# Optimization experiments

Hardware: AMD Instinct MI355X
Metric: run time of the kernel (lower is better)

The kernel has to match this reference:

```python
import jax, jax.numpy as jnp
import numpy as np

EPS = 1e-6

def _quant_per_token(x):
    # dynamic per-token symmetric int8 quantization (simulated in float)
    s = jnp.max(jnp.abs(x), axis=-1, keepdims=True) / 127.0  # [T,1]
    q = jnp.clip(jnp.round(x / s), -127.0, 127.0)
    return q, s

def _quant_weight(W):
    # per-output-channel symmetric int8 weight quantization (W: [out,in])
    s = jnp.max(jnp.abs(W), axis=1, keepdims=True) / 127.0  # [out,1]
    q = jnp.round(W / s)
    return q, s

def _w8a8(qx, sx, W, b):
    # int8xint8 GEMM with per-token act scale and per-channel weight scale, fp out
    qw, sw = _quant_weight(W)
    return (qx @ qw.T) * (sx * sw.T) + b

def _rmsnorm_bias(x, w, b, eps=EPS):
    # RMSNormGeneral: x * rsqrt(mean(x^2)+eps) * w + b (no mean subtraction)
    var = jnp.mean(x * x, axis=-1, keepdims=True)
    return x * jax.lax.rsqrt(var + eps) * w + b

def setup_inputs() -> dict:
    key = jax.random.key(0)
    ks = jax.random.split(key, 16)
    E, H, F = 1280, 20, 5120
    B, S = 16, 1024
    T = B * S
    d = {
        'hidden': jax.random.normal(ks[0], (T, E), jnp.float32),
        'ln1_w': jax.random.uniform(ks[1], (E,), jnp.float32, 0.5, 1.5),
        'ln1_b': jax.random.normal(ks[2], (E,), jnp.float32) * 0.02,
        'ln2_w': jax.random.uniform(ks[3], (E,), jnp.float32, 0.5, 1.5),
        'ln2_b': jax.random.normal(ks[4], (E,), jnp.float32) * 0.02,
        'W_qkv': jax.random.normal(ks[5], (3 * E, E), jnp.float32) * 0.02,
        'b_qkv': jax.random.normal(ks[6], (3 * E,), jnp.float32) * 0.02,
        'W_out': jax.random.normal(ks[7], (E, E), jnp.float32) * 0.02,
        'b_out': jax.random.normal(ks[8], (E,), jnp.float32) * 0.02,
        'W_fc1': jax.random.normal(ks[9], (F, E), jnp.float32) * 0.02,
        'b_fc1': jax.random.normal(ks[10], (F,), jnp.float32) * 0.02,
        'W_fc2': jax.random.normal(ks[11], (E, F), jnp.float32) * 0.02,
        'b_fc2': jax.random.normal(ks[12], (E,), jnp.float32) * 0.02,
        'bsz': B,
        'seqlen': S,
    }
    return d

def reference(hidden, ln1_w, ln1_b, ln2_w, ln2_b, W_qkv, b_qkv, W_out, b_out,
              W_fc1, b_fc1, W_fc2, b_fc2, bsz, seqlen):
    E = hidden.shape[-1]
    H = 20
    hd = E // H

    # --- self-attention block ---
    residual = hidden
    y = _rmsnorm_bias(hidden, ln1_w, ln1_b)
    qx, sx = _quant_per_token(y)
    qkv = _w8a8(qx, sx, W_qkv, b_qkv)                      # [T, 3E]
    q, k, v = jnp.split(qkv, 3, axis=-1)
    q = q.reshape(bsz, seqlen, H, hd)
    k = k.reshape(bsz, seqlen, H, hd)
    v = v.reshape(bsz, seqlen, H, hd)
    scale = 1.0 / np.sqrt(hd)
    scores = jnp.einsum('bqhd,bkhd->bhqk', q, k) * scale   # non-causal
    probs = jax.nn.softmax(scores, axis=-1)
    attn = jnp.einsum('bhqk,bkhd->bqhd', probs, v).reshape(bsz * seqlen, E)
    qa, sa = _quant_per_token(attn)
    o = _w8a8(qa, sa, W_out, b_out)
    hidden = residual + o

    # --- MLP block ---
    residual = hidden
    y = _rmsnorm_bias(hidden, ln2_w, ln2_b)
    qx, sx = _quant_per_token(y)
    f1 = _w8a8(qx, sx, W_fc1, b_fc1)                       # [T, F]
    g = jax.nn.gelu(f1, approximate=False)                 # fused gelu_and_quant
    qg, sg = _quant_per_token(g)
    f2 = _w8a8(qg, sg, W_fc2, b_fc2)
    return residual + f2
```

## Files before the change

kernel.cpp:

```cpp
#include <hip/hip_runtime.h>
#include <hip/hip_bf16.h>
#include <stdint.h>

#define E_DIM 1280
#define F_DIM 5120
#define T_DIM 16384
#define B_SZ  16
#define S_LEN 1024
#define NH    20

typedef int v4i __attribute__((ext_vector_type(4)));
typedef __attribute__((ext_vector_type(8))) short v8s;
typedef __attribute__((ext_vector_type(4))) float v4f;

__device__ __forceinline__ float wred_sum(float v) {
#pragma unroll
  for (int m = 32; m > 0; m >>= 1) v += __shfl_xor(v, m, 64);
  return v;
}
__device__ __forceinline__ float wred_max(float v) {
#pragma unroll
  for (int m = 32; m > 0; m >>= 1) v = fmaxf(v, __shfl_xor(v, m, 64));
  return v;
}
__device__ __forceinline__ void gload_lds16(const void* g, void* l) {
  __builtin_amdgcn_global_load_lds((const __attribute__((address_space(1))) void*)g,
                                   (__attribute__((address_space(3))) void*)l, 16, 0, 0);
}

__global__ __launch_bounds__(256) void wquant_kernel(
    const float* __restrict__ W, int8_t* __restrict__ qw, float* __restrict__ sw, int K) {
  __shared__ float red[4];
  const int row = blockIdx.x;
  const int tid = threadIdx.x;
  const float* wr = W + (size_t)row * K;
  float amax = 0.f;
  for (int c = tid; c < K; c += 256) amax = fmaxf(amax, fabsf(wr[c]));
  amax = wred_max(amax);
  if ((tid & 63) == 0) red[tid >> 6] = amax;
  __syncthreads();
  amax = fmaxf(fmaxf(red[0], red[1]), fmaxf(red[2], red[3]));
  float sc = amax * (1.0f / 127.0f);
  if (tid == 0) sw[row] = sc;
  for (int c = tid; c < K; c += 256) {
    float qv = rintf(wr[c] / sc);
    qw[(size_t)row * K + c] = (int8_t)qv;
  }
}

__global__ __launch_bounds__(256) void rms_quant_kernel(
    const float* __restrict__ x, const float* __restrict__ w, const float* __restrict__ b,
    int8_t* __restrict__ q, float* __restrict__ s) {
  __shared__ float red[4];
  const int row = blockIdx.x;
  const int tid = threadIdx.x;
  const float* xr = x + (size_t)row * E_DIM;
  float vals[5];
  float ss = 0.f;
#pragma unroll
  for (int i = 0; i < 5; ++i) {
    float v = xr[tid + i * 256];
    vals[i] = v; ss += v * v;
  }
  ss = wred_sum(ss);
  if ((tid & 63) == 0) red[tid >> 6] = ss;
  __syncthreads();
  ss = red[0] + red[1] + red[2] + red[3];
  float rstd = rsqrtf(ss * (1.0f / E_DIM) + 1e-6f);
  float y[5]; float amax = 0.f;
#pragma unroll
  for (int i = 0; i < 5; ++i) {
    int c = tid + i * 256;
    float v = vals[i] * rstd * w[c] + b[c];
    y[i] = v;
    amax = fmaxf(amax, fabsf(v));
  }
  amax = wred_max(amax);
  __syncthreads();
  if ((tid & 63) == 0) red[tid >> 6] = amax;
  __syncthreads();
  amax = fmaxf(fmaxf(red[0], red[1]), fmaxf(red[2], red[3]));
  float sc = amax * (1.0f / 127.0f);
  if (tid == 0) s[row] = sc;
#pragma unroll
  for (int i = 0; i < 5; ++i) {
    int c = tid + i * 256;
    float qv = rintf(y[i] / sc);
    qv = fminf(fmaxf(qv, -127.f), 127.f);
    q[(size_t)row * E_DIM + c] = (int8_t)qv;
  }
}

__global__ __launch_bounds__(256) void row_quant_bf_kernel(
    const __hip_bfloat16* __restrict__ x, int8_t* __restrict__ q, float* __restrict__ s) {
  __shared__ float red[4];
  const int row = blockIdx.x;
  const int tid = threadIdx.x;
  const __hip_bfloat16* xr = x + (size_t)row * E_DIM;
  float vals[5]; float amax = 0.f;
#pragma unroll
  for (int i = 0; i < 5; ++i) {
    float v = __bfloat162float(xr[tid + i * 256]);
    vals[i] = v;
    amax = fmaxf(amax, fabsf(v));
  }
  amax = wred_max(amax);
  if ((tid & 63) == 0) red[tid >> 6] = amax;
  __syncthreads();
  amax = fmaxf(fmaxf(red[0], red[1]), fmaxf(red[2], red[3]));
  float sc = amax * (1.0f / 127.0f);
  if (tid == 0) s[row] = sc;
#pragma unroll
  for (int i = 0; i < 5; ++i) {
    int c = tid + i * 256;
    float qv = rintf(vals[i] / sc);
    qv = fminf(fmaxf(qv, -127.f), 127.f);
    q[(size_t)row * E_DIM + c] = (int8_t)qv;
  }
}

__global__ __launch_bounds__(256) void gelu_quant_kernel(
    const __hip_bfloat16* __restrict__ f1, int8_t* __restrict__ q, float* __restrict__ s) {
  __shared__ float red[4];
  const int row = blockIdx.x;
  const int tid = threadIdx.x;
  const __hip_bfloat16* xr = f1 + (size_t)row * F_DIM;
  float g[20]; float amax = 0.f;
#pragma unroll
  for (int i = 0; i < 20; ++i) {
    float v = __bfloat162float(xr[tid + i * 256]);
    float gv = 0.5f * v * (1.0f + erff(v * 0.70710678118654752440f));
    g[i] = gv;
    amax = fmaxf(amax, fabsf(gv));
  }
  amax = wred_max(amax);
  if ((tid & 63) == 0) red[tid >> 6] = amax;
  __syncthreads();
  amax = fmaxf(fmaxf(red[0], red[1]), fmaxf(red[2], red[3]));
  float sc = amax * (1.0f / 127.0f);
  if (tid == 0) s[row] = sc;
  int8_t* qr = q + (size_t)row * (2 * F_DIM);
#pragma unroll
  for (int i = 0; i < 20; ++i) {
    int c = tid + i * 256;
    float qv = rintf(g[i] / sc);
    qv = fminf(fmaxf(qv, -127.f), 127.f);
    qr[c] = (int8_t)qv;
  }
}

template <int MODE>
__global__ __launch_bounds__(512, 2) void gemm256_i8(
    const int8_t* __restrict__ A, const int8_t* __restrict__ B,
    const float* __restrict__ sx, const float* __restrict__ sw,
    const float* __restrict__ bias, const float* __restrict__ resid,
    void* __restrict__ outp, int M, int N, int K, int lda) {
  __shared__ __align__(16) int8_t As[2][2][256 * 64];
  __shared__ __align__(16) int8_t Bs[2][2][256 * 64];

  const int tid = threadIdx.x;
  const int lane = tid & 63;
  const int wave = tid >> 6;
  const int wm = wave >> 2;
  const int wn = wave & 3;
  const int l16 = lane & 15;
  const int quad = lane >> 4;
  const int choff = (quad ^ ((l16 >> 1) & 3)) << 4;

  const int nwg = gridDim.x;
  const int ntn = N >> 8;
  const int u = (blockIdx.x & 7) * (nwg >> 3) + (blockIdx.x >> 3);
  const int tm = u / ntn, tn = u % ntn;
  const int m0 = tm << 8, n0 = tn << 8;

  const int8_t* A_blk = A + (size_t)m0 * lda;
  const int8_t* B_blk = B + (size_t)n0 * K;

  const int r0 = tid >> 2;
  const int sch = ((tid & 3) ^ ((tid >> 3) & 3)) << 4;

#define STAGE_A(KT, DST)                                                         \
  {                                                                              \
    gload_lds16(A_blk + (size_t)r0 * lda + (size_t)(KT)*64 + sch,                \
                (DST) + tid * 16);                                               \
    gload_lds16(A_blk + (size_t)(r0 + 128) * lda + (size_t)(KT)*64 + sch,        \
                (DST) + 8192 + tid * 16);                                        \
  }
#define STAGE_B(KT, DST)                                                         \
  {                                                                              \
    gload_lds16(B_blk + (size_t)r0 * K + (size_t)(KT)*64 + sch,                  \
                (DST) + tid * 16);                                               \
    gload_lds16(B_blk + (size_t)(r0 + 128) * K + (size_t)(KT)*64 + sch,          \
                (DST) + 8192 + tid * 16);                                        \
  }

  v4i acc[8][4];
#pragma unroll
  for (int i = 0; i < 8; ++i)
#pragma unroll
    for (int j = 0; j < 4; ++j) acc[i][j] = (v4i){0, 0, 0, 0};

  const int nk = K >> 6;
  const int niter = nk >> 1;

  STAGE_A(0, &As[0][0][0]); STAGE_B(0, &Bs[0][0][0]);
  STAGE_A(1, &As[0][1][0]); STAGE_B(1, &Bs[0][1][0]);
  asm volatile("s_waitcnt vmcnt(4)" ::: "memory");
  asm volatile("s_barrier" ::: "memory");

#pragma unroll 1
  for (int i = 0; i < niter - 1; ++i) {
    const int pr = i & 1;
    const int kt2 = 2 * i + 2;
#pragma unroll
    for (int ph = 0; ph < 4; ++ph) {
      const int tt = ph >> 1;
      const int qm = ph & 1;
      const int8_t* At = &As[pr][tt][0];
      const int8_t* Bt = &Bs[pr][tt][0];
      v4i af[4], bf[4];
#pragma unroll
      for (int ii = 0; ii < 4; ++ii)
        af[ii] = *(const v4i*)(At + (wm * 128 + qm * 64 + ii * 16 + l16) * 64 + choff);
#pragma unroll
      for (int jj = 0; jj < 4; ++jj)
        bf[jj] = *(const v4i*)(Bt + (wn * 64 + jj * 16 + l16) * 64 + choff);
      if (qm == 0) {
        STAGE_A(kt2 + tt, &As[pr ^ 1][tt][0]);
      } else {
        STAGE_B(kt2 + tt, &Bs[pr ^ 1][tt][0]);
      }
      asm volatile("s_barrier" ::: "memory");
      __builtin_amdgcn_s_setprio(1);
#pragma unroll
      for (int ii = 0; ii < 4; ++ii)
#pragma unroll
        for (int jj = 0; jj < 4; ++jj)
          acc[qm * 4 + ii][jj] = __builtin_amdgcn_mfma_i32_16x16x64_i8(
              af[ii], bf[jj], acc[qm * 4 + ii][jj], 0, 0, 0);
      __builtin_amdgcn_s_setprio(0);
      if (qm == 1) asm volatile("s_waitcnt vmcnt(4)" ::: "memory");
      asm volatile("s_barrier" ::: "memory");
    }
  }

  {
    const int pr = (niter - 1) & 1;
#pragma unroll
    for (int ph = 0; ph < 4; ++ph) {
      const int tt = ph >> 1;
      const int qm = ph & 1;
      const int8_t* At = &As[pr][tt][0];
      const int8_t* Bt = &Bs[pr][tt][0];
      v4i af[4], bf[4];
#pragma unroll
      for (int ii = 0; ii < 4; ++ii)
        af[ii] = *(const v4i*)(At + (wm * 128 + qm * 64 + ii * 16 + l16) * 64 + choff);
#pragma unroll
      for (int jj = 0; jj < 4; ++jj)
        bf[jj] = *(const v4i*)(Bt + (wn * 64 + jj * 16 + l16) * 64 + choff);
      asm volatile("s_barrier" ::: "memory");
      __builtin_amdgcn_s_setprio(1);
#pragma unroll
      for (int ii = 0; ii < 4; ++ii)
#pragma unroll
        for (int jj = 0; jj < 4; ++jj)
          acc[qm * 4 + ii][jj] = __builtin_amdgcn_mfma_i32_16x16x64_i8(
              af[ii], bf[jj], acc[qm * 4 + ii][jj], 0, 0, 0);
      __builtin_amdgcn_s_setprio(0);
      if (ph == 1) asm volatile("s_waitcnt vmcnt(0)" ::: "memory");
      asm volatile("s_barrier" ::: "memory");
    }
  }
#undef STAGE_A
#undef STAGE_B

  float swv[4], bv[4];
#pragma unroll
  for (int jj = 0; jj < 4; ++jj) {
    int n = n0 + wn * 64 + jj * 16 + l16;
    swv[jj] = sw[n];
    bv[jj] = bias[n];
  }
#pragma unroll
  for (int mf = 0; mf < 8; ++mf) {
#pragma unroll
    for (int r = 0; r < 4; ++r) {
      int m = m0 + wm * 128 + mf * 16 + quad * 4 + r;
      float sxm = sx[m];
#pragma unroll
      for (int jj = 0; jj < 4; ++jj) {
        int n = n0 + wn * 64 + jj * 16 + l16;
        float v = (float)acc[mf][jj][r] * (sxm * swv[jj]) + bv[jj];
        if constexpr (MODE == 0) {
          ((__hip_bfloat16*)outp)[(size_t)m * N + n] = __float2bfloat16(v);
        } else {
          ((float*)outp)[(size_t)m * N + n] = v + resid[(size_t)m * N + n];
        }
      }
    }
  }
}

template <int MODE>
__global__ __launch_bounds__(256, 2) void gemm128_i8(
    const int8_t* __restrict__ A, const int8_t* __restrict__ B,
    const float* __restrict__ sx, const float* __restrict__ sw,
    const float* __restrict__ bias, const float* __restrict__ resid,
    void* __restrict__ outp, int M, int N, int K, int lda) {
  __shared__ __align__(16) int8_t As[4][128 * 64];
  __shared__ __align__(16) int8_t Bs[4][128 * 64];

  const int tid = threadIdx.x;
  const int lane = tid & 63;
  const int wave = tid >> 6;
  const int wm = wave >> 1;
  const int wn = wave & 1;
  const int l16 = lane & 15;
  const int quad = lane >> 4;
  const int choff = (quad ^ ((l16 >> 1) & 3)) << 4;

  const int nwg = gridDim.x;
  const int ntn = N >> 7;
  const int u = (blockIdx.x & 7) * (nwg >> 3) + (blockIdx.x >> 3);
  const int tm = u / ntn, tn = u % ntn;
  const int m0 = tm << 7, n0 = tn << 7;

  const int8_t* A_blk = A + (size_t)m0 * lda;
  const int8_t* B_blk = B + (size_t)n0 * K;

  const int r0 = tid >> 2;
  const int sch = ((tid & 3) ^ ((tid >> 3) & 3)) << 4;

#define STAGE_A(KT, SLOT)                                                        \
  {                                                                              \
    gload_lds16(A_blk + (size_t)r0 * lda + (size_t)(KT)*64 + sch,                \
                &As[SLOT][tid * 16]);                                            \
    gload_lds16(A_blk + (size_t)(r0 + 64) * lda + (size_t)(KT)*64 + sch,         \
                &As[SLOT][4096 + tid * 16]);                                     \
  }
#define STAGE_B(KT, SLOT)                                                        \
  {                                                                              \
    gload_lds16(B_blk + (size_t)r0 * K + (size_t)(KT)*64 + sch,                  \
                &Bs[SLOT][tid * 16]);                                            \
    gload_lds16(B_blk + (size_t)(r0 + 64) * K + (size_t)(KT)*64 + sch,           \
                &Bs[SLOT][4096 + tid * 16]);                                     \
  }

#define KTILE(SLOT, STAGE_STMT, WAIT_STMT)                                       \
  {                                                                              \
    const int8_t* At = &As[SLOT][0];                                             \
    const int8_t* Bt = &Bs[SLOT][0];                                             \
    v4i af[4], bf[4];                                                            \
    _Pragma("unroll") for (int ii = 0; ii < 4; ++ii)                             \
        af[ii] = *(const v4i*)(At + (wm * 64 + ii * 16 + l16) * 64 + choff);     \
    _Pragma("unroll") for (int jj = 0; jj < 4; ++jj)                             \
        bf[jj] = *(const v4i*)(Bt + (wn * 64 + jj * 16 + l16) * 64 + choff);     \
    STAGE_STMT;                                                                  \
    asm volatile("s_barrier" ::: "memory");                                      \
    __builtin_amdgcn_s_setprio(1);                                               \
    _Pragma("unroll") for (int ii = 0; ii < 4; ++ii)                             \
        _Pragma("unroll") for (int jj = 0; jj < 4; ++jj)                         \
            acc[ii][jj] = __builtin_amdgcn_mfma_i32_16x16x64_i8(                 \
                af[ii], bf[jj], acc[ii][jj], 0, 0, 0);                           \
    __builtin_amdgcn_s_setprio(0);                                               \
    WAIT_STMT;                                                                   \
    asm volatile("s_barrier" ::: "memory");                                      \
  }

  v4i acc[4][4];
#pragma unroll
  for (int i = 0; i < 4; ++i)
#pragma unroll
    for (int j = 0; j < 4; ++j) acc[i][j] = (v4i){0, 0, 0, 0};

  const int nk = K >> 6;

  STAGE_A(0, 0); STAGE_B(0, 0);
  STAGE_A(1, 1); STAGE_B(1, 1);
  STAGE_A(2, 2); STAGE_B(2, 2);
  asm volatile("s_waitcnt vmcnt(8)" ::: "memory");
  asm volatile("s_barrier" ::: "memory");

#pragma unroll 1
  for (int kt = 0; kt < nk - 3; ++kt) {
    const int sl = kt & 3;
    const int s3 = (kt + 3) & 3;
    KTILE(sl, { STAGE_A(kt + 3, s3); STAGE_B(kt + 3, s3); },
          asm volatile("s_waitcnt vmcnt(8)" ::: "memory"));
  }
  KTILE((nk - 3) & 3, ((void)0), asm volatile("s_waitcnt vmcnt(4)" ::: "memory"));
  KTILE((nk - 2) & 3, ((void)0), asm volatile("s_waitcnt vmcnt(0)" ::: "memory"));
  KTILE((nk - 1) & 3, ((void)0), ((void)0));
#undef KTILE
#undef STAGE_A
#undef STAGE_B

  float swv[4], bv[4];
#pragma unroll
  for (int jj = 0; jj < 4; ++jj) {
    int n = n0 + wn * 64 + jj * 16 + l16;
    swv[jj] = sw[n];
    bv[jj] = bias[n];
  }
#pragma unroll
  for (int ii = 0; ii < 4; ++ii) {
#pragma unroll
    for (int r = 0; r < 4; ++r) {
      int m = m0 + wm * 64 + ii * 16 + quad * 4 + r;
      float sxm = sx[m];
#pragma unroll
      for (int jj = 0; jj < 4; ++jj) {
        int n = n0 + wn * 64 + jj * 16 + l16;
        float v = (float)acc[ii][jj][r] * (sxm * swv[jj]) + bv[jj];
        if constexpr (MODE == 0) {
          ((__hip_bfloat16*)outp)[(size_t)m * N + n] = __float2bfloat16(v);
        } else {
          ((float*)outp)[(size_t)m * N + n] = v + resid[(size_t)m * N + n];
        }
      }
    }
  }
}

__global__ __launch_bounds__(256) void vt_kernel(
    const __hip_bfloat16* __restrict__ qkv, __hip_bfloat16* __restrict__ Vt) {
  __shared__ __hip_bfloat16 tile[64][72];
  const int bh = blockIdx.y, kc = blockIdx.x;
  const int b = bh / NH, h = bh % NH;
  const int tid = threadIdx.x;
  const size_t base = ((size_t)b * S_LEN + (size_t)kc * 64) * (3 * E_DIM) + 2 * E_DIM + h * 64;
#pragma unroll
  for (int i = 0; i < 2; ++i) {
    int idx = tid + i * 256;
    int row = idx >> 3, c8 = (idx & 7) * 8;
    *(uint4*)&tile[row][c8] = *(const uint4*)(qkv + base + (size_t)row * (3 * E_DIM) + c8);
  }
  __syncthreads();
#pragma unroll
  for (int i = 0; i < 2; ++i) {
    int idx = tid + i * 256;
    int d = idx >> 3, k8 = (idx & 7) * 8;
    __hip_bfloat16 v[8] __attribute__((aligned(16)));
#pragma unroll
    for (int j = 0; j < 8; ++j) v[j] = tile[k8 + j][d];
    *(uint4*)&Vt[((size_t)bh * 64 + d) * 1024 + (size_t)kc * 64 + k8] = *(uint4*)v;
  }
}

__global__ __launch_bounds__(256) void attn_flash_kernel(
    const __hip_bfloat16* __restrict__ qkv, const __hip_bfloat16* __restrict__ Vt,
    __hip_bfloat16* __restrict__ attn) {
  constexpr int E3 = 3 * E_DIM;
  __shared__ __align__(16) __hip_bfloat16 Ks[128 * 64];
  __shared__ __align__(16) __hip_bfloat16 Vs[64 * 128];
  __shared__ __align__(16) __hip_bfloat16 Ps[4][16 * 128];
  __shared__ float stats[4][16];

  const int tid = threadIdx.x;
  const int lane = tid & 63;
  const int wave = tid >> 6;
  const int l16 = lane & 15;
  const int quad = lane >> 4;
  const int bh = blockIdx.y;
  const int b = bh / NH, h = bh % NH;
  const int q0 = blockIdx.x * 64;
  const size_t base_t = (size_t)b * S_LEN;

  v8s qb0, qb1;
  {
    const __hip_bfloat16* qp =
        qkv + (base_t + q0 + wave * 16 + l16) * (size_t)E3 + h * 64 + quad * 8;
    qb0 = *(const v8s*)qp;
    qb1 = *(const v8s*)(qp + 32);
  }

  float m_prev = -3.0e38f;
  float lsum = 0.f;
  v4f oc[4];
#pragma unroll
  for (int dt = 0; dt < 4; ++dt) oc[dt] = (v4f){0.f, 0.f, 0.f, 0.f};

  const __hip_bfloat16* kgbase = qkv + base_t * E3 + E_DIM + h * 64;
  const __hip_bfloat16* vgbase = Vt + (size_t)bh * 64 * 1024;
  __hip_bfloat16* pw = Ps[wave];

#pragma unroll 1
  for (int t = 0; t < 8; ++t) {
    __syncthreads();
#pragma unroll
    for (int i = 0; i < 4; ++i) {
      int c = tid + i * 256;
      int row = c >> 3, lc = c & 7;
      int gc = lc ^ (row & 7);
      gload_lds16(kgbase + (size_t)(t * 128 + row) * E3 + gc * 8, (char*)Ks + c * 16);
    }
#pragma unroll
    for (int i = 0; i < 4; ++i) {
      int c = tid + i * 256;
      int d = c >> 4, lc = c & 15;
      int gc = lc ^ (d & 15);
      gload_lds16(vgbase + (size_t)d * 1024 + t * 128 + gc * 8, (char*)Vs + c * 16);
    }
    __syncthreads();

    v4f accT[8];
#pragma unroll
    for (int nt = 0; nt < 8; ++nt) {
      int row = nt * 16 + l16;
      const char* kr = (const char*)Ks + row * 128;
      v8s ak0 = *(const v8s*)(kr + ((quad ^ (row & 7)) * 16));
      v8s ak1 = *(const v8s*)(kr + (((quad + 4) ^ (row & 7)) * 16));
      v4f z = {0.f, 0.f, 0.f, 0.f};
      z = __builtin_amdgcn_mfma_f32_16x16x32_bf16(ak0, qb0, z, 0, 0, 0);
      accT[nt] = __builtin_amdgcn_mfma_f32_16x16x32_bf16(ak1, qb1, accT[nt] = z, 0, 0, 0);
    }

    float mt = -3.0e38f;
#pragma unroll
    for (int nt = 0; nt < 8; ++nt)
#pragma unroll
      for (int r = 0; r < 4; ++r) mt = fmaxf(mt, accT[nt][r]);
    mt = fmaxf(mt, __shfl_xor(mt, 16, 64));
    mt = fmaxf(mt, __shfl_xor(mt, 32, 64));
    float m_new = fmaxf(m_prev, mt);
    float alpha = __expf(0.125f * (m_prev - m_new));
    m_prev = m_new;
    float ts = 0.f;
#pragma unroll
    for (int nt = 0; nt < 8; ++nt)
#pragma unroll
      for (int r = 0; r < 4; ++r) {
        float e = __expf(0.125f * (accT[nt][r] - m_new));
        accT[nt][r] = e;
        ts += e;
      }
    lsum = lsum * alpha + ts;
    if (quad == 0) stats[wave][l16] = alpha;
#pragma unroll
    for (int nt = 0; nt < 8; ++nt) {
      __hip_bfloat16 pk[4] __attribute__((aligned(8)));
#pragma unroll
      for (int r = 0; r < 4; ++r) pk[r] = __float2bfloat16(accT[nt][r]);
      int lcq = 2 * nt + (quad >> 1);
      *(uint2*)((char*)pw + l16 * 256 + ((lcq ^ l16) * 16) + (quad & 1) * 8) = *(uint2*)pk;
    }
    v4f a4 = *(v4f*)&stats[wave][quad * 4];
#pragma unroll
    for (int dt = 0; dt < 4; ++dt)
#pragma unroll
      for (int r = 0; r < 4; ++r) oc[dt][r] *= a4[r];
#pragma unroll
    for (int ks = 0; ks < 4; ++ks) {
      int pch = (ks * 4 + quad) ^ l16;
      v8s ap = *(const v8s*)((char*)pw + l16 * 256 + pch * 16);
#pragma unroll
      for (int dt = 0; dt < 4; ++dt) {
        int d = dt * 16 + l16;
        v8s bv = *(const v8s*)((char*)Vs + d * 256 + (((ks * 4 + quad) ^ l16) * 16));
        oc[dt] = __builtin_amdgcn_mfma_f32_16x16x32_bf16(ap, bv, oc[dt], 0, 0, 0);
      }
    }
  }

  lsum += __shfl_xor(lsum, 16, 64);
  lsum += __shfl_xor(lsum, 32, 64);
  if (quad == 0) stats[wave][l16] = lsum;
  v4f l4 = *(v4f*)&stats[wave][quad * 4];
  float inv[4];
#pragma unroll
  for (int r = 0; r < 4; ++r) inv[r] = 1.0f / l4[r];
#pragma unroll
  for (int dt = 0; dt < 4; ++dt)
#pragma unroll
    for (int r = 0; r < 4; ++r) {
      int tok = q0 + wave * 16 + quad * 4 + r;
      attn[(base_t + tok) * (size_t)E_DIM + h * 64 + dt * 16 + l16] =
          __float2bfloat16(oc[dt][r] * inv[r]);
    }
}

extern "C" void kernel_launch(void* const* d_in, const int* in_sizes, int n_in,
                              void* d_out, int out_size, void* d_ws, size_t ws_size,
                              hipStream_t stream) {
  const float* hidden = (const float*)d_in[0];
  const float* ln1_w = (const float*)d_in[1];
  const float* ln1_b = (const float*)d_in[2];
  const float* ln2_w = (const float*)d_in[3];
  const float* ln2_b = (const float*)d_in[4];
  const float* W_qkv = (const float*)d_in[5];
  const float* b_qkv = (const float*)d_in[6];
  const float* W_out = (const float*)d_in[7];
  const float* b_out = (const float*)d_in[8];
  const float* W_fc1 = (const float*)d_in[9];
  const float* b_fc1 = (const float*)d_in[10];
  const float* W_fc2 = (const float*)d_in[11];
  const float* b_fc2 = (const float*)d_in[12];

  char* ws = (char*)d_ws;
  size_t off = 0;
  auto alloc = [&](size_t bytes) {
    void* p = ws + off;
    off += (bytes + 255) & ~(size_t)255;
    return p;
  };
  int8_t* qw_qkv = (int8_t*)alloc((size_t)3 * E_DIM * E_DIM);
  int8_t* qw_out = (int8_t*)alloc((size_t)E_DIM * E_DIM);
  int8_t* qw_fc1 = (int8_t*)alloc((size_t)F_DIM * E_DIM);
  int8_t* qw_fc2 = (int8_t*)alloc((size_t)E_DIM * F_DIM);
  float* sw_qkv = (float*)alloc((size_t)3 * E_DIM * 4);
  float* sw_out = (float*)alloc((size_t)E_DIM * 4);
  float* sw_fc1 = (float*)alloc((size_t)F_DIM * 4);
  float* sw_fc2 = (float*)alloc((size_t)E_DIM * 4);
  float* sx1 = (float*)alloc((size_t)T_DIM * 4);
  float* sa  = (float*)alloc((size_t)T_DIM * 4);
  float* sx2 = (float*)alloc((size_t)T_DIM * 4);
  float* sg  = (float*)alloc((size_t)T_DIM * 4);
  int8_t* qx = (int8_t*)alloc((size_t)T_DIM * E_DIM);
  char* R = (char*)alloc((size_t)T_DIM * 3 * E_DIM * 2 +
                         (size_t)T_DIM * E_DIM * 4);
  __hip_bfloat16* qkv_bf = (__hip_bfloat16*)R;
  __hip_bfloat16* attn_bf = (__hip_bfloat16*)(R + (size_t)T_DIM * 3 * E_DIM * 2);
  __hip_bfloat16* Vt = (__hip_bfloat16*)(R + (size_t)T_DIM * 3 * E_DIM * 2 +
                                         (size_t)T_DIM * E_DIM * 2);
  __hip_bfloat16* f1_bf = (__hip_bfloat16*)R;
  int8_t* qg = (int8_t*)R;
  float* hidden2 = (float*)d_out;

  wquant_kernel<<<3 * E_DIM, 256, 0, stream>>>(W_qkv, qw_qkv, sw_qkv, E_DIM);
  wquant_kernel<<<E_DIM, 256, 0, stream>>>(W_out, qw_out, sw_out, E_DIM);
  wquant_kernel<<<F_DIM, 256, 0, stream>>>(W_fc1, qw_fc1, sw_fc1, E_DIM);
  wquant_kernel<<<E_DIM, 256, 0, stream>>>(W_fc2, qw_fc2, sw_fc2, F_DIM);
  rms_quant_kernel<<<T_DIM, 256, 0, stream>>>(hidden, ln1_w, ln1_b, qx, sx1);
  gemm256_i8<0><<<(T_DIM / 256) * (3 * E_DIM / 256), 512, 0, stream>>>(
      qx, qw_qkv, sx1, sw_qkv, b_qkv, nullptr, qkv_bf, T_DIM, 3 * E_DIM, E_DIM, E_DIM);
  vt_kernel<<<dim3(S_LEN / 64, B_SZ * NH), 256, 0, stream>>>(qkv_bf, Vt);
  attn_flash_kernel<<<dim3(S_LEN / 64, B_SZ * NH), 256, 0, stream>>>(qkv_bf, Vt, attn_bf);
  row_quant_bf_kernel<<<T_DIM, 256, 0, stream>>>(attn_bf, qx, sa);
  gemm128_i8<1><<<(T_DIM / 128) * (E_DIM / 128), 256, 0, stream>>>(
      qx, qw_out, sa, sw_out, b_out, hidden, hidden2, T_DIM, E_DIM, E_DIM, E_DIM);
  rms_quant_kernel<<<T_DIM, 256, 0, stream>>>(hidden2, ln2_w, ln2_b, qx, sx2);
  gemm256_i8<0><<<(T_DIM / 256) * (F_DIM / 256), 512, 0, stream>>>(
      qx, qw_fc1, sx2, sw_fc1, b_fc1, nullptr, f1_bf, T_DIM, F_DIM, E_DIM, E_DIM);
  gelu_quant_kernel<<<T_DIM, 256, 0, stream>>>(f1_bf, qg, sg);
  gemm128_i8<1><<<(T_DIM / 128) * (E_DIM / 128), 256, 0, stream>>>(
      qg, qw_fc2, sg, sw_fc2, b_fc2, hidden2, (float*)d_out, T_DIM, E_DIM, F_DIM, 2 * F_DIM);
}
```

Before: 1.041 ms.

## Prefetch K/V tiles via registers, remap blocks for XCD locality, lazy softmax rescale

The flash-attention kernel now loads the next K/V tile into registers while the current tile is computed, then writes it to LDS after the MFMA work, so global latency overlaps with compute. The launch becomes a 1D grid remapped so that consecutive heads/query tiles land on the same XCD, which should improve L2 reuse of K/V. Softmax uses exp2 with a prefolded scale, and the running-max rescale of the accumulators is skipped unless the max grows by more than a threshold. s_setprio hints are wrapped around the MFMA sections. The register staging raises VGPR pressure, and the lazy rescale depends on the values staying within a bounded exponent range.

```diff
diff --git a/kernel.cpp b/kernel.cpp
--- a/kernel.cpp
+++ b/kernel.cpp
@@ -462,9 +462,10 @@
   const int wave = tid >> 6;
   const int l16 = lane & 15;
   const int quad = lane >> 4;
-  const int bh = blockIdx.y;
+  const int wg = (blockIdx.x & 7) * 640 + (blockIdx.x >> 3);
+  const int bh = wg >> 4;
   const int b = bh / NH, h = bh % NH;
-  const int q0 = blockIdx.x * 64;
+  const int q0 = (wg & 15) * 64;
   const size_t base_t = (size_t)b * S_LEN;
 
   v8s qb0, qb1;
@@ -475,36 +476,53 @@
     qb1 = *(const v8s*)(qp + 32);
   }
 
-  float m_prev = -3.0e38f;
-  float lsum = 0.f;
-  v4f oc[4];
-#pragma unroll
-  for (int dt = 0; dt < 4; ++dt) oc[dt] = (v4f){0.f, 0.f, 0.f, 0.f};
-
   const __hip_bfloat16* kgbase = qkv + base_t * E3 + E_DIM + h * 64;
   const __hip_bfloat16* vgbase = Vt + (size_t)bh * 64 * 1024;
   __hip_bfloat16* pw = Ps[wave];
 
+  const __hip_bfloat16* ksrc[4];
+  const __hip_bfloat16* vsrc[4];
+  int cdst[4];
+#pragma unroll
+  for (int i = 0; i < 4; ++i) {
+    int c = tid + i * 256;
+    cdst[i] = c * 16;
+    int row = c >> 3, lc = c & 7;
+    int gc = lc ^ (row & 7);
+    ksrc[i] = kgbase + (size_t)row * E3 + gc * 8;
+    int d = c >> 4, lcv = c & 15;
+    int gv = lcv ^ (d & 15);
+    vsrc[i] = vgbase + (size_t)d * 1024 + gv * 8;
+  }
+
+#pragma unroll
+  for (int i = 0; i < 4; ++i) gload_lds16(ksrc[i], (char*)Ks + cdst[i]);
+#pragma unroll
+  for (int i = 0; i < 4; ++i) gload_lds16(vsrc[i], (char*)Vs + cdst[i]);
+  __syncthreads();
+
+  constexpr float CEXP = 0.18033688011112042f;
+  float m_prev = -3.0e38f;
+  float mc = m_prev * CEXP;
+  float lsum = 0.f;
+  v4f oc[4];
+#pragma unroll
+  for (int dt = 0; dt < 4; ++dt) oc[dt] = (v4f){0.f, 0.f, 0.f, 0.f};
+
 #pragma unroll 1
   for (int t = 0; t < 8; ++t) {
-    __syncthreads();
-#pragma unroll
-    for (int i = 0; i < 4; ++i) {
-      int c = tid + i * 256;
-      int row = c >> 3, lc = c & 7;
-      int gc = lc ^ (row & 7);
-      gload_lds16(kgbase + (size_t)(t * 128 + row) * E3 + gc * 8, (char*)Ks + c * 16);
-    }
-#pragma unroll
-    for (int i = 0; i < 4; ++i) {
-      int c = tid + i * 256;
-      int d = c >> 4, lc = c & 15;
-      int gc = lc ^ (d & 15);
-      gload_lds16(vgbase + (size_t)d * 1024 + t * 128 + gc * 8, (char*)Vs + c * 16);
-    }
-    __syncthreads();
+    v4i kreg[4], vreg[4];
+    if (t < 7) {
+#pragma unroll
+      for (int i = 0; i < 4; ++i)
+        kreg[i] = *(const v4i*)(ksrc[i] + (size_t)(t + 1) * 128 * E3);
+#pragma unroll
+      for (int i = 0; i < 4; ++i)
+        vreg[i] = *(const v4i*)(vsrc[i] + (size_t)(t + 1) * 128);
+    }
 
     v4f accT[8];
+    __builtin_amdgcn_s_setprio(1);
 #pragma unroll
     for (int nt = 0; nt < 8; ++nt) {
       int row = nt * 16 + l16;
@@ -515,28 +533,39 @@
       z = __builtin_amdgcn_mfma_f32_16x16x32_bf16(ak0, qb0, z, 0, 0, 0);
       accT[nt] = __builtin_amdgcn_mfma_f32_16x16x32_bf16(ak1, qb1, accT[nt] = z, 0, 0, 0);
     }
+    __builtin_amdgcn_s_setprio(0);
 
     float mt = -3.0e38f;
 #pragma unroll
     for (int nt = 0; nt < 8; ++nt)
-#pragma unroll
-      for (int r = 0; r < 4; ++r) mt = fmaxf(mt, accT[nt][r]);
+      mt = fmaxf(mt, fmaxf(fmaxf(accT[nt][0], accT[nt][1]),
+                           fmaxf(accT[nt][2], accT[nt][3])));
     mt = fmaxf(mt, __shfl_xor(mt, 16, 64));
     mt = fmaxf(mt, __shfl_xor(mt, 32, 64));
-    float m_new = fmaxf(m_prev, mt);
-    float alpha = __expf(0.125f * (m_prev - m_new));
-    m_prev = m_new;
+    if (__any(mt > m_prev + 48.0f)) {
+      float m_new = fmaxf(m_prev, mt);
+      float mcn = m_new * CEXP;
+      float alpha = exp2f(m_prev * CEXP - mcn);
+      m_prev = m_new;
+      mc = mcn;
+      lsum *= alpha;
+      if (quad == 0) stats[wave][l16] = alpha;
+      v4f a4 = *(v4f*)&stats[wave][quad * 4];
+#pragma unroll
+      for (int dt = 0; dt < 4; ++dt)
+#pragma unroll
+        for (int r = 0; r < 4; ++r) oc[dt][r] *= a4[r];
+    }
     float ts = 0.f;
 #pragma unroll
     for (int nt = 0; nt < 8; ++nt)
 #pragma unroll
       for (int r = 0; r < 4; ++r) {
-        float e = __expf(0.125f * (accT[nt][r] - m_new));
+        float e = exp2f(fmaf(accT[nt][r], CEXP, -mc));
         accT[nt][r] = e;
         ts += e;
       }
-    lsum = lsum * alpha + ts;
-    if (quad == 0) stats[wave][l16] = alpha;
+    lsum += ts;
 #pragma unroll
     for (int nt = 0; nt < 8; ++nt) {
       __hip_bfloat16 pk[4] __attribute__((aligned(8)));
@@ -545,11 +574,7 @@
       int lcq = 2 * nt + (quad >> 1);
       *(uint2*)((char*)pw + l16 * 256 + ((lcq ^ l16) * 16) + (quad & 1) * 8) = *(uint2*)pk;
     }
-    v4f a4 = *(v4f*)&stats[wave][quad * 4];
-#pragma unroll
-    for (int dt = 0; dt < 4; ++dt)
-#pragma unroll
-      for (int r = 0; r < 4; ++r) oc[dt][r] *= a4[r];
+    __builtin_amdgcn_s_setprio(1);
 #pragma unroll
     for (int ks = 0; ks < 4; ++ks) {
       int pch = (ks * 4 + quad) ^ l16;
@@ -561,6 +586,16 @@
         oc[dt] = __builtin_amdgcn_mfma_f32_16x16x32_bf16(ap, bv, oc[dt], 0, 0, 0);
       }
     }
+    __builtin_amdgcn_s_setprio(0);
+
+    __syncthreads();
+    if (t < 7) {
+#pragma unroll
+      for (int i = 0; i < 4; ++i) *(v4i*)((char*)Ks + cdst[i]) = kreg[i];
+#pragma unroll
+      for (int i = 0; i < 4; ++i) *(v4i*)((char*)Vs + cdst[i]) = vreg[i];
+    }
+    __syncthreads();
   }
 
   lsum += __shfl_xor(lsum, 16, 64);
@@ -635,7 +670,7 @@
   gemm256_i8<0><<<(T_DIM / 256) * (3 * E_DIM / 256), 512, 0, stream>>>(
       qx, qw_qkv, sx1, sw_qkv, b_qkv, nullptr, qkv_bf, T_DIM, 3 * E_DIM, E_DIM, E_DIM);
   vt_kernel<<<dim3(S_LEN / 64, B_SZ * NH), 256, 0, stream>>>(qkv_bf, Vt);
-  attn_flash_kernel<<<dim3(S_LEN / 64, B_SZ * NH), 256, 0, stream>>>(qkv_bf, Vt, attn_bf);
+  attn_flash_kernel<<<(S_LEN / 64) * B_SZ * NH, 256, 0, stream>>>(qkv_bf, Vt, attn_bf);
   row_quant_bf_kernel<<<T_DIM, 256, 0, stream>>>(attn_bf, qx, sa);
   gemm128_i8<1><<<(T_DIM / 128) * (E_DIM / 128), 256, 0, stream>>>(
       qx, qw_out, sa, sw_out, b_out, hidden, hidden2, T_DIM, E_DIM, E_DIM, E_DIM);
```

New measurement: 1.045 ms. About the same (+0.4%).
